# Kernel optimization log

Hardware: AMD Instinct MI355X
Metric: run time of the kernel (lower is better)

Reference implementation:

```python
import jax, jax.numpy as jnp
import numpy as np

V, E, H, B, T = 50000, 300, 512, 256, 64
D_OUT = 3
EPS = 1e-5


def setup_inputs() -> dict:
    key = jax.random.key(0)
    ks = jax.random.split(key, 16)
    s = lambda k, shape: (jax.random.normal(k, shape, jnp.float32) * 0.05)
    return {
        "premise": jax.random.randint(ks[0], (T, B), 0, V),
        "hypothesis": jax.random.randint(ks[1], (T, B), 0, V),
        "embed": s(ks[2], (V, E)),
        "W_ih": s(ks[3], (4 * H, E)),
        "W_hh": s(ks[4], (4 * H, H)),
        "b_ih": s(ks[5], (4 * H,)),
        "b_hh": s(ks[6], (4 * H,)),
        "bn0_g": jnp.ones((4 * H,), jnp.float32),
        "bn0_b": jnp.zeros((4 * H,), jnp.float32),
        "W0": s(ks[7], (4 * H, 4 * H)),
        "b0": s(ks[8], (4 * H,)),
        "bn1_g": jnp.ones((4 * H,), jnp.float32),
        "bn1_b": jnp.zeros((4 * H,), jnp.float32),
        "W1": s(ks[9], (4 * H, 4 * H)),
        "b1": s(ks[10], (4 * H,)),
        "bno_g": jnp.ones((4 * H,), jnp.float32),
        "bno_b": jnp.zeros((4 * H,), jnp.float32),
        "Wo": s(ks[11], (D_OUT, 4 * H)),
        "bo": s(ks[12], (D_OUT,)),
    }


def _lstm_final_h(xs, W_ih, W_hh, bias):
    # xs: [T, N, E]; shared-weight LSTMCell scan, returns final hidden [N, H]
    x_proj = jnp.einsum('tne,ge->tng', xs, W_ih) + bias  # hoist input GEMM out of the recurrence
    n = xs.shape[1]
    h0 = jnp.zeros((n, H), xs.dtype)

    def step(carry, xg):
        h, c = carry
        gates = xg + h @ W_hh.T
        i, f, g, o = jnp.split(gates, 4, axis=-1)  # torch LSTMCell gate order
        c = jax.nn.sigmoid(f) * c + jax.nn.sigmoid(i) * jnp.tanh(g)
        h = jax.nn.sigmoid(o) * jnp.tanh(c)
        return (h, c), None

    (h, _), _ = jax.lax.scan(step, (h0, h0), x_proj)
    return h


def _bn(x, g, b):
    # BatchNorm1d in training mode: biased batch stats
    mu = x.mean(0)
    var = x.var(0)
    return (x - mu) * jax.lax.rsqrt(var + EPS) * g + b


def reference(premise, hypothesis, embed, W_ih, W_hh, b_ih, b_hh,
              bn0_g, bn0_b, W0, b0, bn1_g, bn1_b, W1, b1,
              bno_g, bno_b, Wo, bo):
    p = embed[premise]      # [T, B, E]
    hyp = embed[hypothesis]  # [T, B, E]
    combined = jnp.concatenate([p, hyp], axis=1)  # [T, 2B, E]
    bias = b_ih + b_hh
    h_fw = _lstm_final_h(combined, W_ih, W_hh, bias)          # forward direction
    h_bw = _lstm_final_h(combined[::-1], W_ih, W_hh, bias)    # backward direction (shared cell)
    feat = jnp.concatenate([h_fw[:B], h_bw[:B], h_fw[B:], h_bw[B:]], axis=1)  # [B, 4H]
    x = jax.nn.relu(_bn(feat, bn0_g, bn0_b) @ W0.T + b0)
    x = jax.nn.relu(_bn(x, bn1_g, bn1_b) @ W1.T + b1)
    return _bn(x, bno_g, bno_b) @ Wo.T + bo  # [B, d_out]
```

## Files before the change

kernel.cpp:

```cpp
#include <hip/hip_runtime.h>
#include <hip/hip_bf16.h>


typedef __attribute__((ext_vector_type(8))) short bf16x8;
typedef __attribute__((ext_vector_type(4))) float f32x4;
typedef __attribute__((ext_vector_type(2))) unsigned int u32x2;

#define DEVI __device__ __forceinline__

template<int N> struct IC { static constexpr int v = N; };

template<int AUX> DEVI void async16t(const void* g, void* l) {
  __builtin_amdgcn_global_load_lds((const __attribute__((address_space(1))) void*)g,
                                   (__attribute__((address_space(3))) void*)l,
                                   16, 0, AUX);
}
DEVI void async16(const void* g, void* l) { async16t<0>(g, l); }
DEVI u32x2 load8_pin(const void* addr) {
  u32x2 r;
  asm volatile("global_load_dwordx2 %0, %1, off" : "=v"(r) : "v"(addr) : "memory");
  return r;
}
DEVI void storeh_coh(void* a, unsigned int v) {
  asm volatile("global_store_short %0, %1, off sc0 sc1" ::"v"(a), "v"(v) : "memory");
}
template<int N> DEVI void vmwait_barrier() {
  asm volatile("s_waitcnt vmcnt(%0)" ::"i"(N) : "memory");
  __builtin_amdgcn_s_barrier();
  __builtin_amdgcn_sched_barrier(0);
}
DEVI float sigmf_(float x) { return 1.f / (1.f + __expf(-x)); }
DEVI float tanhf_(float x) {
  float a = __expf(-2.f * fabsf(x));
  float t = (1.f - a) / (1.f + a);
  return copysignf(t, x);
}
DEVI __hip_bfloat16 f2b(float x) { return __float2bfloat16(x); }
DEVI float b2f(__hip_bfloat16 x) { return __bfloat162float(x); }

__global__ void cvt_f32_bf16(const float* __restrict__ src,
                             __hip_bfloat16* __restrict__ dst, int n4) {
  int i = blockIdx.x * 256 + threadIdx.x;
  int stride = gridDim.x * 256;
  for (; i < n4; i += stride) {
    float4 v = ((const float4*)src)[i];
    union { __hip_bfloat16 h[4]; uint2 u; } o;
    o.h[0] = f2b(v.x); o.h[1] = f2b(v.y); o.h[2] = f2b(v.z); o.h[3] = f2b(v.w);
    ((uint2*)dst)[i] = o.u;
  }
}

__global__ void pack_wih(const float* __restrict__ W_ih,
                         const float* __restrict__ b_ih,
                         const float* __restrict__ b_hh,
                         __hip_bfloat16* __restrict__ WihP,
                         float* __restrict__ biasL) {
  int tid = blockIdx.x * 256 + threadIdx.x;
  int stride = gridDim.x * 256;
  for (int i = tid; i < 2048 * 320; i += stride) {
    int r = i / 320, c = i - r * 320;
    WihP[i] = (c < 300) ? f2b(W_ih[r * 300 + c]) : f2b(0.f);
  }
  if (tid < 2048) biasL[tid] = b_ih[tid] + b_hh[tid];
}

__global__ void gather_kernel(const int* __restrict__ prem, const int* __restrict__ hyp,
                              const float* __restrict__ embed,
                              __hip_bfloat16* __restrict__ Ain) {
  int row = blockIdx.x * 4 + (threadIdx.x >> 6);
  int lane = threadIdx.x & 63;
  int tt = row >> 9, n = row & 511;
  int tok = (n < 256) ? prem[tt * 256 + n] : hyp[tt * 256 + (n - 256)];
  const float4* e4 = (const float4*)(embed + (size_t)tok * 300);
  uint2* d2 = (uint2*)(Ain + (size_t)row * 320);
  for (int j = lane; j < 75; j += 64) {
    float4 v = e4[j];
    union { __hip_bfloat16 h[4]; uint2 u; } o;
    o.h[0] = f2b(v.x); o.h[1] = f2b(v.y); o.h[2] = f2b(v.z); o.h[3] = f2b(v.w);
    d2[j] = o.u;
  }
  for (int j = 75 + lane; j < 80; j += 64) d2[j] = make_uint2(0u, 0u);
}

template<int BM, int EPI>
__global__ __launch_bounds__(256)
void gemm_pipe(const __hip_bfloat16* __restrict__ A,
               const __hip_bfloat16* __restrict__ Bn,
               const float* __restrict__ bias,
               void* __restrict__ Cout, int K, int ldc) {
  constexpr int BK = 64;
  constexpr int ABYT = BM * BK * 2;
  constexpr int BBYT = 128 * BK * 2;
  constexpr int APW = BM / 32;
  constexpr int IFL = APW + 4;
  constexpr int WM = BM / 2, MT = WM / 16;
  __shared__ alignas(16) char smem[2 * ABYT + 2 * BBYT];

  const int tid = threadIdx.x, lane = tid & 63, wid = tid >> 6;
  const int wrow = wid >> 1, wcol = wid & 1;
  const int m0 = blockIdx.x * BM, n0 = blockIdx.y * 128;
  const int l8 = lane & 7, ld8 = lane >> 3;
  const int swz = (l8 ^ ld8) * 8;

  const __hip_bfloat16* Abase = A + (size_t)m0 * K;
  const __hip_bfloat16* Bbase = Bn + (size_t)n0 * K;

  f32x4 acc[MT][4];
#pragma unroll
  for (int i = 0; i < MT; ++i)
#pragma unroll
    for (int j = 0; j < 4; ++j) acc[i][j] = {0.f, 0.f, 0.f, 0.f};

  auto stage = [&](int buf, int kt) {
    const __hip_bfloat16* as = Abase + kt * BK + swz;
    char* ad = smem + buf * ABYT;
#pragma unroll
    for (int s = 0; s < APW; ++s) {
      int iss = wid * APW + s;
      async16(as + (size_t)(iss * 8 + ld8) * K, ad + iss * 1024);
    }
    const __hip_bfloat16* bs = Bbase + kt * BK + swz;
    char* bd = smem + 2 * ABYT + buf * BBYT;
#pragma unroll
    for (int s = 0; s < 4; ++s) {
      int iss = wid * 4 + s;
      async16(bs + (size_t)(iss * 8 + ld8) * K, bd + iss * 1024);
    }
  };

  const int nk = K / BK;
  stage(0, 0);
  for (int kt = 0; kt < nk; ++kt) {
    if (kt + 1 < nk) {
      stage((kt + 1) & 1, kt + 1);
      vmwait_barrier<IFL>();
    } else {
      vmwait_barrier<0>();
    }
    const __hip_bfloat16* ab = (const __hip_bfloat16*)(smem + (kt & 1) * ABYT);
    const __hip_bfloat16* bb = (const __hip_bfloat16*)(smem + 2 * ABYT + (kt & 1) * BBYT);
#pragma unroll
    for (int kk = 0; kk < BK; kk += 32) {
      bf16x8 af[MT], bf[4];
#pragma unroll
      for (int i = 0; i < MT; ++i) {
        int r = wrow * WM + i * 16 + (lane & 15);
        af[i] = *(const bf16x8*)&ab[r * BK + ((kk + (lane >> 4) * 8) ^ ((r & 7) * 8))];
      }
#pragma unroll
      for (int j = 0; j < 4; ++j) {
        int r = wcol * 64 + j * 16 + (lane & 15);
        bf[j] = *(const bf16x8*)&bb[r * BK + ((kk + (lane >> 4) * 8) ^ ((r & 7) * 8))];
      }
#pragma unroll
      for (int i = 0; i < MT; ++i)
#pragma unroll
        for (int j = 0; j < 4; ++j)
          acc[i][j] = __builtin_amdgcn_mfma_f32_16x16x32_bf16(af[i], bf[j], acc[i][j], 0, 0, 0);
    }
    __builtin_amdgcn_s_barrier();
  }

  if (EPI == 2) {
#pragma unroll
    for (int i = 0; i < MT; ++i)
#pragma unroll
      for (int j = 0; j < 4; ++j) {
        union { __hip_bfloat16 h[4]; uint2 u; } o;
#pragma unroll
        for (int rr = 0; rr < 4; ++rr) o.h[rr] = f2b(acc[i][j][rr]);
        size_t slot = (((size_t)blockIdx.x * 16 + blockIdx.y) * 4 + wid) * 16 + i * 4 + j;
        *(uint2*)((char*)Cout + slot * 512 + lane * 8) = o.u;
      }
    return;
  }

  __syncthreads();
  float* Csm = (float*)smem;
#pragma unroll
  for (int i = 0; i < MT; ++i)
#pragma unroll
    for (int j = 0; j < 4; ++j)
#pragma unroll
      for (int rr = 0; rr < 4; ++rr) {
        int row = wrow * WM + i * 16 + (lane >> 4) * 4 + rr;
        int col = wcol * 64 + j * 16 + (lane & 15);
        Csm[row * 128 + (col ^ ((row & 7) << 2))] = acc[i][j][rr];
      }
  __syncthreads();
#pragma unroll
  for (int it = 0; it < BM / 16; ++it) {
    int idx = it * 256 + tid;
    int row = idx >> 4;
    int cb = (idx & 15) * 8;
    int sw = (row & 7) << 2;
    float4 v0 = *(const float4*)&Csm[row * 128 + (cb ^ sw)];
    float4 v1 = *(const float4*)&Csm[row * 128 + ((cb + 4) ^ sw)];
    float4 b0 = *(const float4*)&bias[n0 + cb];
    float4 b1 = *(const float4*)&bias[n0 + cb + 4];
    v0.x = fmaxf(v0.x + b0.x, 0.f); v0.y = fmaxf(v0.y + b0.y, 0.f);
    v0.z = fmaxf(v0.z + b0.z, 0.f); v0.w = fmaxf(v0.w + b0.w, 0.f);
    v1.x = fmaxf(v1.x + b1.x, 0.f); v1.y = fmaxf(v1.y + b1.y, 0.f);
    v1.z = fmaxf(v1.z + b1.z, 0.f); v1.w = fmaxf(v1.w + b1.w, 0.f);
    size_t base = (size_t)(m0 + row) * ldc + n0 + cb;
    *(float4*)&((float*)Cout)[base] = v0;
    *(float4*)&((float*)Cout)[base + 4] = v1;
  }
}

__global__ __launch_bounds__(256, 2)
void lstm_persist(const __hip_bfloat16* __restrict__ xp,
                  const __hip_bfloat16* __restrict__ Whh,
                  const float* __restrict__ biasL,
                  __hip_bfloat16* __restrict__ hA,
                  __hip_bfloat16* __restrict__ hB,
                  int* __restrict__ ctr) {
  extern __shared__ char smem[];
  const int tid = threadIdx.x, lane = tid & 63, wid = tid >> 6;
  const int bid = blockIdx.x;
  const int gi = (bid & 7) | ((bid >> 7) << 3);
  const int jt = (bid >> 3) & 15;
  const int gl = (gi < 16) ? gi : gi - 16;
  const int m0 = (gi < 16) ? gi * 32 : 512 + gl * 32;
  const int l8 = lane & 7, ld8 = lane >> 3;
  const int swz = (l8 ^ ld8) * 8;

  bf16x8 w[2][16];
#pragma unroll
  for (int kt = 0; kt < 8; ++kt) {
#pragma unroll
    for (int s = 0; s < 4; ++s) {
      int lr32 = s * 8 + ld8;
      int Wrow = wid * 512 + jt * 32 + lr32;
      async16(Whh + (size_t)Wrow * 512 + kt * 64 + swz,
              smem + wid * 4096 + s * 1024);
    }
    asm volatile("s_waitcnt vmcnt(0)" ::: "memory");
    __builtin_amdgcn_s_barrier();
    __builtin_amdgcn_sched_barrier(0);
    {
      const __hip_bfloat16* wb = (const __hip_bfloat16*)(smem + wid * 4096);
#pragma unroll
      for (int j = 0; j < 2; ++j) {
        int r = j * 16 + (lane & 15);
#pragma unroll
        for (int kkh = 0; kkh < 2; ++kkh)
          w[j][kt * 2 + kkh] =
              *(const bf16x8*)&wb[r * 64 + ((kkh * 32 + (lane >> 4) * 8) ^ ((r & 7) * 8))];
      }
    }
    __syncthreads();
  }

  int* flag = (int*)(smem + 49152);
  if (tid == 0) {
    int xcd = (int)(__builtin_amdgcn_s_getreg((31 << 11) | 20) & 15);
    int o1 = atomicOr(&ctr[512 + gi], 1 << xcd);
    int o2 = atomicOr(&ctr[561], 1 << xcd);
    asm volatile("" ::"v"(o1), "v"(o2));
    atomicAdd(&ctr[560], 1);
    while (__hip_atomic_load(&ctr[560], __ATOMIC_RELAXED, __HIP_MEMORY_SCOPE_AGENT) < 512)
      __builtin_amdgcn_s_sleep(2);
    int gm = __hip_atomic_load(&ctr[512 + gi], __ATOMIC_RELAXED, __HIP_MEMORY_SCOPE_AGENT);
    int am = __hip_atomic_load(&ctr[561], __ATOMIC_RELAXED, __HIP_MEMORY_SCOPE_AGENT);
    *flag = (__popc((unsigned)gm) == 1 && __popc((unsigned)am) == 8) ? 1 : 0;
  }
  __syncthreads();
  const bool fastpath = (*flag != 0);
  __syncthreads();

  const int rq = tid >> 5;
  const int col = tid & 31;
  const int i_x = (gl & 1) * 2 + (rq >> 2);
  const int wid_x = ((gl & 3) >> 1) * 2 + ((jt & 3) >> 1);
  const int j_x = (jt & 1) * 2 + (col >> 4);
  const int lane_x = ((rq & 3) << 4) | (col & 15);

  float bias_[4];
#pragma unroll
  for (int g = 0; g < 4; ++g) bias_[g] = biasL[g * 512 + jt * 32 + col];

  float c_[4];
#pragma unroll
  for (int e = 0; e < 4; ++e) c_[e] = 0.f;

  auto run = [&](auto FC) {
    constexpr bool FAST = decltype(FC)::v;
    constexpr int AUX = FAST ? 1 : 17;
    for (int t = 0; t < 64; ++t) {
      const __hip_bfloat16* hin = (t & 1) ? hB : hA;
      __hip_bfloat16* hout = (t & 1) ? hA : hB;

      const int TT = (gi < 16) ? t : 63 - t;
      const int bx = TT * 4 + (gl >> 2);
      u32x2 xg[4];
#pragma unroll
      for (int g = 0; g < 4; ++g) {
        int by = g * 4 + (jt >> 2);
        size_t slot = (((size_t)bx * 16 + by) * 4 + wid_x) * 16 + i_x * 4 + j_x;
        xg[g] = load8_pin((const char*)xp + slot * 512 + lane_x * 8);
      }
      __builtin_amdgcn_sched_barrier(0);

      if (t > 0) {
        if (wid == 0) {
          bool ok;
          do {
            int v = __hip_atomic_load(&ctr[gi * 16 + (lane & 15)], __ATOMIC_RELAXED,
                                      __HIP_MEMORY_SCOPE_AGENT);
            ok = __all(v >= t);
            if (!ok) __builtin_amdgcn_s_sleep(1);
          } while (!ok);
        }
        __syncthreads();
      }

#pragma unroll
      for (int kt = 0; kt < 8; ++kt)
        async16t<AUX>(hin + (size_t)(m0 + wid * 8 + ld8) * 512 + kt * 64 + swz,
                      smem + kt * 4096 + wid * 1024);
      __builtin_amdgcn_sched_barrier(0);

      f32x4 acc[2][2];
#pragma unroll
      for (int i = 0; i < 2; ++i)
#pragma unroll
        for (int j = 0; j < 2; ++j) acc[i][j] = {0.f, 0.f, 0.f, 0.f};

      auto do_kt = [&](int kt) {
        const __hip_bfloat16* ab = (const __hip_bfloat16*)(smem + kt * 4096);
#pragma unroll
        for (int kk = 0; kk < 64; kk += 32) {
          bf16x8 af[2];
#pragma unroll
          for (int i = 0; i < 2; ++i) {
            int r = i * 16 + (lane & 15);
            af[i] = *(const bf16x8*)&ab[r * 64 + ((kk + (lane >> 4) * 8) ^ ((r & 7) * 8))];
          }
#pragma unroll
          for (int i = 0; i < 2; ++i)
#pragma unroll
            for (int j = 0; j < 2; ++j)
              acc[i][j] = __builtin_amdgcn_mfma_f32_16x16x32_bf16(
                  af[i], w[j][kt * 2 + kk / 32], acc[i][j], 0, 0, 0);
        }
      };
      vmwait_barrier<4>();
#pragma unroll
      for (int kt = 0; kt < 4; ++kt) do_kt(kt);
      vmwait_barrier<0>();
#pragma unroll
      for (int kt = 4; kt < 8; ++kt) do_kt(kt);

      float* gsm = (float*)(smem + 32768);
      __syncthreads();
#pragma unroll
      for (int i = 0; i < 2; ++i)
#pragma unroll
        for (int j = 0; j < 2; ++j)
          *(f32x4*)(gsm + (wid * 4 + i * 2 + j) * 256 + lane * 4) = acc[i][j];
      __syncthreads();
      f32x4 gq[4];
      {
        const int iq = rq >> 2, jq = col >> 4;
        const int lprime = ((rq & 3) << 4) | (col & 15);
#pragma unroll
        for (int g = 0; g < 4; ++g)
          gq[g] = *(const f32x4*)(gsm + (g * 4 + iq * 2 + jq) * 256 + lprime * 4);
      }

      union { u32x2 v; __hip_bfloat16 h[4]; } X[4];
#pragma unroll
      for (int g = 0; g < 4; ++g) X[g].v = xg[g];
      __hip_bfloat16* hbase = hout + (size_t)(m0 + rq * 4) * 512 + jt * 32 + col;
#pragma unroll
      for (int rr = 0; rr < 4; ++rr) {
        float gi_ = gq[0][rr] + b2f(X[0].h[rr]) + bias_[0];
        float gf = gq[1][rr] + b2f(X[1].h[rr]) + bias_[1];
        float gg = gq[2][rr] + b2f(X[2].h[rr]) + bias_[2];
        float go = gq[3][rr] + b2f(X[3].h[rr]) + bias_[3];
        float cn = sigmf_(gf) * c_[rr] + sigmf_(gi_) * tanhf_(gg);
        float hn = sigmf_(go) * tanhf_(cn);
        c_[rr] = cn;
        union { __hip_bfloat16 b; unsigned short u; } hb;
        hb.b = f2b(hn);
        if constexpr (FAST) {
          hbase[rr * 512] = hb.b;
        } else {
          storeh_coh(hbase + rr * 512, (unsigned int)hb.u);
        }
      }
      asm volatile("s_waitcnt vmcnt(0)" ::: "memory");
      __syncthreads();
      if (tid == 0)
        __hip_atomic_store(&ctr[gi * 16 + jt], t + 1, __ATOMIC_RELAXED,
                           __HIP_MEMORY_SCOPE_AGENT);
    }
  };
  if (fastpath) run(IC<1>{});
  else          run(IC<0>{});
}

__global__ void feat_kernel(const __hip_bfloat16* __restrict__ hA, float* __restrict__ feat) {
  int b = blockIdx.x;
  for (int c = threadIdx.x; c < 2048; c += 256) {
    int sec = c >> 9, j = c & 511;
    int row = (sec == 0) ? b : (sec == 1) ? 512 + b : (sec == 2) ? 256 + b : 768 + b;
    feat[b * 2048 + c] = b2f(hA[(size_t)row * 512 + j]);
  }
}

__global__ void bn_stats(const float* __restrict__ x, const float* __restrict__ g,
                         const float* __restrict__ b,
                         float* __restrict__ sc, float* __restrict__ sh) {
  int c = blockIdx.x * 256 + threadIdx.x;
  float s = 0.f, s2 = 0.f;
  for (int r = 0; r < 256; ++r) {
    float v = x[r * 2048 + c];
    s += v;
    s2 += v * v;
  }
  float mu = s * (1.f / 256.f);
  float var = s2 * (1.f / 256.f) - mu * mu;
  float rs = rsqrtf(var + 1e-5f);
  float scale = g[c] * rs;
  sc[c] = scale;
  sh[c] = b[c] - mu * scale;
}

__global__ void bn_apply(const float* __restrict__ x, const float* __restrict__ sc,
                         const float* __restrict__ sh, __hip_bfloat16* __restrict__ xn) {
  int i = blockIdx.x * 256 + threadIdx.x;
  int c = i & 2047;
  xn[i] = f2b(x[i] * sc[c] + sh[c]);
}

__global__ void final_kernel(const float* __restrict__ x2, const float* __restrict__ sc,
                             const float* __restrict__ sh, const float* __restrict__ Wo,
                             const float* __restrict__ bo, float* __restrict__ out) {
  __shared__ float red[3][256];
  int b = blockIdx.x, tid = threadIdx.x;
  float a0 = 0.f, a1 = 0.f, a2 = 0.f;
  for (int c = tid; c < 2048; c += 256) {
    float v = x2[b * 2048 + c] * sc[c] + sh[c];
    a0 += v * Wo[c];
    a1 += v * Wo[2048 + c];
    a2 += v * Wo[4096 + c];
  }
  red[0][tid] = a0; red[1][tid] = a1; red[2][tid] = a2;
  __syncthreads();
  for (int s = 128; s > 0; s >>= 1) {
    if (tid < s) {
      red[0][tid] += red[0][tid + s];
      red[1][tid] += red[1][tid + s];
      red[2][tid] += red[2][tid + s];
    }
    __syncthreads();
  }
  if (tid < 3) out[b * 3 + tid] = red[tid][0] + bo[tid];
}

extern "C" void kernel_launch(void* const* d_in, const int* in_sizes, int n_in,
                              void* d_out, int out_size, void* d_ws, size_t ws_size,
                              hipStream_t stream) {
  (void)in_sizes; (void)n_in; (void)out_size; (void)ws_size;
  const int* prem = (const int*)d_in[0];
  const int* hyp = (const int*)d_in[1];
  const float* embed = (const float*)d_in[2];
  const float* W_ih = (const float*)d_in[3];
  const float* W_hh = (const float*)d_in[4];
  const float* b_ih = (const float*)d_in[5];
  const float* b_hh = (const float*)d_in[6];
  const float* bn0g = (const float*)d_in[7];
  const float* bn0b = (const float*)d_in[8];
  const float* W0 = (const float*)d_in[9];
  const float* b0 = (const float*)d_in[10];
  const float* bn1g = (const float*)d_in[11];
  const float* bn1b = (const float*)d_in[12];
  const float* W1 = (const float*)d_in[13];
  const float* b1 = (const float*)d_in[14];
  const float* bnog = (const float*)d_in[15];
  const float* bnob = (const float*)d_in[16];
  const float* Wo = (const float*)d_in[17];
  const float* bo = (const float*)d_in[18];
  float* out = (float*)d_out;

  char* w = (char*)d_ws;
  size_t off = 0;
  auto alloc = [&](size_t bytes) {
    void* p = w + off;
    off += (bytes + 255) & ~(size_t)255;
    return p;
  };
  __hip_bfloat16* WihP = (__hip_bfloat16*)alloc((size_t)2048 * 320 * 2);
  __hip_bfloat16* Whhb = (__hip_bfloat16*)alloc((size_t)2048 * 512 * 2);
  __hip_bfloat16* W0b = (__hip_bfloat16*)alloc((size_t)2048 * 2048 * 2);
  __hip_bfloat16* W1b = (__hip_bfloat16*)alloc((size_t)2048 * 2048 * 2);
  float* biasL = (float*)alloc(2048 * 4);
  int* ctr = (int*)alloc(1024 * 4);
  __hip_bfloat16* xp = (__hip_bfloat16*)alloc((size_t)32768 * 2048 * 2);
  size_t ain_off = off;
  __hip_bfloat16* Ain = (__hip_bfloat16*)alloc((size_t)32768 * 320 * 2);
  size_t end_off = off;
  off = ain_off;
  __hip_bfloat16* hA = (__hip_bfloat16*)alloc((size_t)1024 * 512 * 2);
  __hip_bfloat16* hB = (__hip_bfloat16*)alloc((size_t)1024 * 512 * 2);
  float* feat = (float*)alloc((size_t)256 * 2048 * 4);
  __hip_bfloat16* xn = (__hip_bfloat16*)alloc((size_t)256 * 2048 * 2);
  float* x1 = (float*)alloc((size_t)256 * 2048 * 4);
  float* x2 = (float*)alloc((size_t)256 * 2048 * 4);
  float* sc0 = (float*)alloc(2048 * 4);
  float* sh0 = (float*)alloc(2048 * 4);
  float* sc1 = (float*)alloc(2048 * 4);
  float* sh1 = (float*)alloc(2048 * 4);
  float* sc2 = (float*)alloc(2048 * 4);
  float* sh2 = (float*)alloc(2048 * 4);
  (void)end_off;

  (void)hipMemsetAsync(ctr, 0, 1024 * 4, stream);
  pack_wih<<<512, 256, 0, stream>>>(W_ih, b_ih, b_hh, WihP, biasL);
  cvt_f32_bf16<<<1024, 256, 0, stream>>>(W_hh, Whhb, 2048 * 512 / 4);
  cvt_f32_bf16<<<2048, 256, 0, stream>>>(W0, W0b, 2048 * 2048 / 4);
  cvt_f32_bf16<<<2048, 256, 0, stream>>>(W1, W1b, 2048 * 2048 / 4);
  gather_kernel<<<8192, 256, 0, stream>>>(prem, hyp, embed, Ain);
  gemm_pipe<128, 2><<<dim3(256, 16), 256, 0, stream>>>(Ain, WihP, biasL, xp, 320, 2048);
  (void)hipMemsetAsync(hA, 0, (size_t)1024 * 512 * 2, stream);
  (void)hipFuncSetAttribute(reinterpret_cast<const void*>(lstm_persist),
                            hipFuncAttributeMaxDynamicSharedMemorySize, 65536);
  lstm_persist<<<512, 256, 49408, stream>>>(xp, Whhb, biasL, hA, hB, ctr);
  feat_kernel<<<256, 256, 0, stream>>>(hA, feat);
  bn_stats<<<8, 256, 0, stream>>>(feat, bn0g, bn0b, sc0, sh0);
  bn_apply<<<2048, 256, 0, stream>>>(feat, sc0, sh0, xn);
  gemm_pipe<64, 1><<<dim3(4, 16), 256, 0, stream>>>(xn, W0b, b0, x1, 2048, 2048);
  bn_stats<<<8, 256, 0, stream>>>(x1, bn1g, bn1b, sc1, sh1);
  bn_apply<<<2048, 256, 0, stream>>>(x1, sc1, sh1, xn);
  gemm_pipe<64, 1><<<dim3(4, 16), 256, 0, stream>>>(xn, W1b, b1, x2, 2048, 2048);
  bn_stats<<<8, 256, 0, stream>>>(x2, bnog, bnob, sc2, sh2);
  final_kernel<<<256, 256, 0, stream>>>(x2, sc2, sh2, Wo, bo, out);
}
```

Baseline: 461.7 us.

## Use hardware rcp in activations, fuse weight packing, swap grid order, widen xp stores

Several small changes. Sigmoid and tanh now use an inline v_rcp_f32 in place of IEEE division. The W_hh conversion is folded into the W_ih packing kernel, removing one launch. The GEMM grid is transposed so blockIdx.x walks the N tiles, letting consecutive blocks share the same A rows. The bf16 projection output is stored as 16-byte pairs of MFMA tiles, and the LSTM loader's slot math is adjusted to match. The approximate reciprocal slightly changes activation precision.

```diff
diff --git a/kernel.cpp b/kernel.cpp
--- a/kernel.cpp
+++ b/kernel.cpp
@@ -29,11 +29,15 @@
   __builtin_amdgcn_s_barrier();
   __builtin_amdgcn_sched_barrier(0);
 }
-DEVI float sigmf_(float x) { return 1.f / (1.f + __expf(-x)); }
+DEVI float rcp_(float x) {
+  float r;
+  asm("v_rcp_f32 %0, %1" : "=v"(r) : "v"(x));
+  return r;
+}
+DEVI float sigmf_(float x) { return rcp_(1.f + __expf(-x)); }
 DEVI float tanhf_(float x) {
   float a = __expf(-2.f * fabsf(x));
-  float t = (1.f - a) / (1.f + a);
-  return copysignf(t, x);
+  return copysignf((1.f - a) * rcp_(1.f + a), x);
 }
 DEVI __hip_bfloat16 f2b(float x) { return __float2bfloat16(x); }
 DEVI float b2f(__hip_bfloat16 x) { return __bfloat162float(x); }
@@ -50,16 +54,24 @@
   }
 }
 
-__global__ void pack_wih(const float* __restrict__ W_ih,
-                         const float* __restrict__ b_ih,
-                         const float* __restrict__ b_hh,
-                         __hip_bfloat16* __restrict__ WihP,
-                         float* __restrict__ biasL) {
+__global__ void pack_weights(const float* __restrict__ W_ih,
+                             const float* __restrict__ W_hh,
+                             const float* __restrict__ b_ih,
+                             const float* __restrict__ b_hh,
+                             __hip_bfloat16* __restrict__ WihP,
+                             __hip_bfloat16* __restrict__ Whhb,
+                             float* __restrict__ biasL) {
   int tid = blockIdx.x * 256 + threadIdx.x;
   int stride = gridDim.x * 256;
   for (int i = tid; i < 2048 * 320; i += stride) {
     int r = i / 320, c = i - r * 320;
     WihP[i] = (c < 300) ? f2b(W_ih[r * 300 + c]) : f2b(0.f);
+  }
+  for (int i = tid; i < 2048 * 512 / 4; i += stride) {
+    float4 v = ((const float4*)W_hh)[i];
+    union { __hip_bfloat16 h[4]; uint2 u; } o;
+    o.h[0] = f2b(v.x); o.h[1] = f2b(v.y); o.h[2] = f2b(v.z); o.h[3] = f2b(v.w);
+    ((uint2*)Whhb)[i] = o.u;
   }
   if (tid < 2048) biasL[tid] = b_ih[tid] + b_hh[tid];
 }
@@ -98,7 +110,8 @@
 
   const int tid = threadIdx.x, lane = tid & 63, wid = tid >> 6;
   const int wrow = wid >> 1, wcol = wid & 1;
-  const int m0 = blockIdx.x * BM, n0 = blockIdx.y * 128;
+  const int bx = blockIdx.y, by = blockIdx.x;
+  const int m0 = bx * BM, n0 = by * 128;
   const int l8 = lane & 7, ld8 = lane >> 3;
   const int swz = (l8 ^ ld8) * 8;
 
@@ -165,12 +178,15 @@
 #pragma unroll
     for (int i = 0; i < MT; ++i)
 #pragma unroll
-      for (int j = 0; j < 4; ++j) {
-        union { __hip_bfloat16 h[4]; uint2 u; } o;
-#pragma unroll
-        for (int rr = 0; rr < 4; ++rr) o.h[rr] = f2b(acc[i][j][rr]);
-        size_t slot = (((size_t)blockIdx.x * 16 + blockIdx.y) * 4 + wid) * 16 + i * 4 + j;
-        *(uint2*)((char*)Cout + slot * 512 + lane * 8) = o.u;
+      for (int jp = 0; jp < 2; ++jp) {
+        union { __hip_bfloat16 h[8]; uint4 u; } o;
+#pragma unroll
+        for (int rr = 0; rr < 4; ++rr) {
+          o.h[rr] = f2b(acc[i][2 * jp][rr]);
+          o.h[4 + rr] = f2b(acc[i][2 * jp + 1][rr]);
+        }
+        size_t slotP = (((size_t)bx * 16 + by) * 4 + wid) * 8 + i * 2 + jp;
+        *(uint4*)((char*)Cout + slotP * 1024 + lane * 16) = o.u;
       }
     return;
   }
@@ -297,8 +313,8 @@
 #pragma unroll
       for (int g = 0; g < 4; ++g) {
         int by = g * 4 + (jt >> 2);
-        size_t slot = (((size_t)bx * 16 + by) * 4 + wid_x) * 16 + i_x * 4 + j_x;
-        xg[g] = load8_pin((const char*)xp + slot * 512 + lane_x * 8);
+        size_t slotP = (((size_t)bx * 16 + by) * 4 + wid_x) * 8 + i_x * 2 + (j_x >> 1);
+        xg[g] = load8_pin((const char*)xp + slotP * 1024 + lane_x * 16 + (j_x & 1) * 8);
       }
       __builtin_amdgcn_sched_barrier(0);
 
@@ -518,12 +534,11 @@
   (void)end_off;
 
   (void)hipMemsetAsync(ctr, 0, 1024 * 4, stream);
-  pack_wih<<<512, 256, 0, stream>>>(W_ih, b_ih, b_hh, WihP, biasL);
-  cvt_f32_bf16<<<1024, 256, 0, stream>>>(W_hh, Whhb, 2048 * 512 / 4);
+  pack_weights<<<512, 256, 0, stream>>>(W_ih, W_hh, b_ih, b_hh, WihP, Whhb, biasL);
   cvt_f32_bf16<<<2048, 256, 0, stream>>>(W0, W0b, 2048 * 2048 / 4);
   cvt_f32_bf16<<<2048, 256, 0, stream>>>(W1, W1b, 2048 * 2048 / 4);
   gather_kernel<<<8192, 256, 0, stream>>>(prem, hyp, embed, Ain);
-  gemm_pipe<128, 2><<<dim3(256, 16), 256, 0, stream>>>(Ain, WihP, biasL, xp, 320, 2048);
+  gemm_pipe<128, 2><<<dim3(16, 256), 256, 0, stream>>>(Ain, WihP, biasL, xp, 320, 2048);
   (void)hipMemsetAsync(hA, 0, (size_t)1024 * 512 * 2, stream);
   (void)hipFuncSetAttribute(reinterpret_cast<const void*>(lstm_persist),
                             hipFuncAttributeMaxDynamicSharedMemorySize, 65536);
@@ -531,10 +546,10 @@
   feat_kernel<<<256, 256, 0, stream>>>(hA, feat);
   bn_stats<<<8, 256, 0, stream>>>(feat, bn0g, bn0b, sc0, sh0);
   bn_apply<<<2048, 256, 0, stream>>>(feat, sc0, sh0, xn);
-  gemm_pipe<64, 1><<<dim3(4, 16), 256, 0, stream>>>(xn, W0b, b0, x1, 2048, 2048);
+  gemm_pipe<64, 1><<<dim3(16, 4), 256, 0, stream>>>(xn, W0b, b0, x1, 2048, 2048);
   bn_stats<<<8, 256, 0, stream>>>(x1, bn1g, bn1b, sc1, sh1);
   bn_apply<<<2048, 256, 0, stream>>>(x1, sc1, sh1, xn);
-  gemm_pipe<64, 1><<<dim3(4, 16), 256, 0, stream>>>(xn, W1b, b1, x2, 2048, 2048);
+  gemm_pipe<64, 1><<<dim3(16, 4), 256, 0, stream>>>(xn, W1b, b1, x2, 2048, 2048);
   bn_stats<<<8, 256, 0, stream>>>(x2, bnog, bnob, sc2, sh2);
   final_kernel<<<256, 256, 0, stream>>>(x2, sc2, sh2, Wo, bo, out);
 }
```

After: 442.9 us, median of 2. 4.1% less time.
